# Kernel optimization log

Hardware: AMD Instinct MI355X
Metric: run time of the kernel (lower is better)

The kernel has to match this reference:

```python
import jax, jax.numpy as jnp
import numpy as np
from jax import lax

NUM_HEADS = 6
LN_EPS = 1e-5


def _ln(x, g, b):
    mu = jnp.mean(x, axis=-1, keepdims=True)
    var = jnp.mean(jnp.square(x - mu), axis=-1, keepdims=True)
    return (x - mu) * jax.lax.rsqrt(var + LN_EPS) * g + b


def _gelu(x):
    return jax.nn.gelu(x, approximate=False)


def setup_inputs() -> dict:
    key = jax.random.key(0)
    ks = jax.random.split(key, 16)
    B, N, C = 16, 1025, 384
    hid = 4 * C  # 1536
    k3 = 3  # depthwise kernel size
    s = 0.02
    rn = lambda k, shape: (jax.random.normal(k, shape, jnp.float32) * s)
    return {
        "x": jax.random.normal(ks[0], (B, N, C), jnp.float32),
        "ln1_g": jnp.ones((C,), jnp.float32),
        "ln1_b": jnp.zeros((C,), jnp.float32),
        "qkv_w": rn(ks[1], (3 * C, C)),
        "proj_w": rn(ks[2], (C, C)),
        "proj_b": jnp.zeros((C,), jnp.float32),
        "ln2_g": jnp.ones((C,), jnp.float32),
        "ln2_b": jnp.zeros((C,), jnp.float32),
        "conv1_w": rn(ks[3], (hid, C)),          # 1x1 conv as matrix
        "conv1_b": jnp.zeros((hid,), jnp.float32),
        "conv2_w": rn(ks[4], (hid, 1, k3, k3)),   # depthwise OIHW
        "conv2_b": jnp.zeros((hid,), jnp.float32),
        "conv3_w": rn(ks[5], (C, hid)),           # 1x1 conv as matrix
        "conv3_b": jnp.zeros((C,), jnp.float32),
        "bn1_s": jnp.ones((hid,), jnp.float32), "bn1_b": jnp.zeros((hid,), jnp.float32),
        "bn2_s": jnp.ones((hid,), jnp.float32), "bn2_b": jnp.zeros((hid,), jnp.float32),
        "bn3_s": jnp.ones((C,), jnp.float32), "bn3_b": jnp.zeros((C,), jnp.float32),
        "comp_w": rn(ks[6], (C // 4, C)), "comp_b": jnp.zeros((C // 4,), jnp.float32),
        "exc_w": rn(ks[7], (C, C // 4)), "exc_b": jnp.zeros((C,), jnp.float32),
    }


def _block(x, ln1_g, ln1_b, qkv_w, proj_w, proj_b, ln2_g, ln2_b,
           conv1_w, conv1_b, conv2_w, conv2_b, conv3_w, conv3_b,
           bn1_s, bn1_b, bn2_s, bn2_b, bn3_s, bn3_b,
           comp_w, comp_b, exc_w, exc_b):
    B, N, C = x.shape
    Hh = NUM_HEADS
    hd = C // Hh
    S = int(np.sqrt(N - 1))

    # ---- Attention (manual softmax(QK^T)V) ----
    h = _ln(x, ln1_g, ln1_b)
    qkv = jnp.einsum('bnc,dc->bnd', h, qkv_w).reshape(B, N, 3, Hh, hd)
    qkv = qkv.transpose(2, 0, 3, 1, 4)  # [3,B,H,N,hd]
    q, k, v = qkv[0], qkv[1], qkv[2]
    attn = jax.nn.softmax(jnp.einsum('bhqd,bhkd->bhqk', q, k) * (hd ** -0.5), axis=-1)
    o = jnp.einsum('bhqk,bhkd->bhqd', attn, v).transpose(0, 2, 1, 3).reshape(B, N, C)
    o = o @ proj_w.T + proj_b
    x = x + o

    # ---- DAFF FFN (conv + BN(eval affine) + GELU + SE gating on cls) ----
    h2 = _ln(x, ln2_g, ln2_b)
    cls_tok, tok = h2[:, :1], h2[:, 1:]
    t = tok.reshape(B, S, S, C).transpose(0, 3, 1, 2)  # NCHW
    hid = conv1_w.shape[0]
    y = jnp.einsum('bchw,oc->bohw', t, conv1_w) + conv1_b[None, :, None, None]
    y = y * bn1_s[None, :, None, None] + bn1_b[None, :, None, None]
    y = _gelu(y)
    shortcut = y
    y = lax.conv_general_dilated(y, conv2_w, (1, 1), 'SAME',
                                 feature_group_count=hid,
                                 dimension_numbers=('NCHW', 'OIHW', 'NCHW'))
    y = y + conv2_b[None, :, None, None]
    y = y * bn2_s[None, :, None, None] + bn2_b[None, :, None, None]
    y = shortcut + _gelu(y)
    y = jnp.einsum('bchw,oc->bohw', y, conv3_w) + conv3_b[None, :, None, None]
    y = y * bn3_s[None, :, None, None] + bn3_b[None, :, None, None]
    # SE gate on cls token
    w = jnp.mean(y, axis=(2, 3)).reshape(B, 1, C)
    w = _gelu(w @ comp_w.T + comp_b) @ exc_w.T + exc_b
    cls_out = cls_tok * w
    tok_out = y.reshape(B, C, S * S).transpose(0, 2, 1)
    out = jnp.concatenate([cls_out, tok_out], axis=1)
    return x + out


def reference(x, ln1_g, ln1_b, qkv_w, proj_w, proj_b, ln2_g, ln2_b,
              conv1_w, conv1_b, conv2_w, conv2_b, conv3_w, conv3_b,
              bn1_s, bn1_b, bn2_s, bn2_b, bn3_s, bn3_b,
              comp_w, comp_b, exc_w, exc_b):
    return _block(x, ln1_g, ln1_b, qkv_w, proj_w, proj_b, ln2_g, ln2_b,
                  conv1_w, conv1_b, conv2_w, conv2_b, conv3_w, conv3_b,
                  bn1_s, bn1_b, bn2_s, bn2_b, bn3_s, bn3_b,
                  comp_w, comp_b, exc_w, exc_b)
```

## Files before the change

kernel.cpp:

```cpp
#include <hip/hip_runtime.h>
#include <math.h>

#define DI __device__ __forceinline__

namespace {

constexpr int B_ = 16;
constexpr int N_ = 1025;
constexpr int C_ = 384;
constexpr int H_ = 6;
constexpr int HD_ = 64;
constexpr int HID_ = 1536;
constexpr int P_ = 1024;
constexpr int MTOK = B_ * P_;
constexpr int MALL = B_ * N_;
constexpr int NPAD = 1088;
constexpr long long AF = (long long)MALL * C_;

constexpr int NQKV = 3 * C_ * C_;
constexpr int NPROJ = C_ * C_;
constexpr int NC1 = HID_ * C_;
constexpr int NC3 = C_ * HID_;
constexpr int NW2 = HID_ * 9;
constexpr int T1 = NQKV, T2 = T1 + NPROJ, T3 = T2 + NC1, T4 = T3 + NC3;
constexpr int T5 = T4 + NW2, T6 = T5 + HID_;

typedef __attribute__((ext_vector_type(4))) float f32x4;
typedef __attribute__((ext_vector_type(8))) short bf16x8;

DI float gelu_f(float x) { return 0.5f * x * (1.0f + erff(x * 0.7071067811865475f)); }

DI float us2f(unsigned short u) {
  union { unsigned int i; float f; } c; c.i = ((unsigned)u) << 16; return c.f;
}
DI unsigned short f2us(float f) {
  union { float f; unsigned int i; } c; c.f = f;
  unsigned int r = c.i + 0x7FFF + ((c.i >> 16) & 1);
  return (unsigned short)(r >> 16);
}
DI unsigned short f2us_trunc(float f) {
  union { float f; unsigned int i; } c; c.f = f;
  return (unsigned short)(c.i >> 16);
}
DI void bf8_to_f(const uint4 v, float* f) {
  const unsigned int u[4] = {v.x, v.y, v.z, v.w};
#pragma unroll
  for (int t = 0; t < 4; t++) {
    union { unsigned int i; float fl; } lo, hi;
    lo.i = (u[t] & 0xffffu) << 16;
    hi.i = u[t] & 0xffff0000u;
    f[2 * t] = lo.fl; f[2 * t + 1] = hi.fl;
  }
}
DI uint4 f_to_bf8(const float* f) {
  unsigned int w[4];
#pragma unroll
  for (int t = 0; t < 4; t++)
    w[t] = (unsigned)f2us(f[2 * t]) | ((unsigned)f2us(f[2 * t + 1]) << 16);
  return make_uint4(w[0], w[1], w[2], w[3]);
}

DI void gl2lds16(const unsigned short* g, unsigned short* l) {
  __builtin_amdgcn_global_load_lds(
      (const __attribute__((address_space(1))) void*)g,
      (__attribute__((address_space(3))) void*)l, 16, 0, 0);
}

__global__ __launch_bounds__(256) void cvtall_kernel(
    const float* __restrict__ qkv_w, const float* __restrict__ proj_w,
    const float* __restrict__ conv1_w, const float* __restrict__ conv3_w,
    const float* __restrict__ conv2_w, const float* __restrict__ c2b,
    const float* __restrict__ s2, const float* __restrict__ b2,
    unsigned short* __restrict__ dst16, float* __restrict__ Bc)
{
  const int idx = blockIdx.x * 256 + threadIdx.x;
  if (idx < T1)      dst16[idx] = f2us(qkv_w[idx]);
  else if (idx < T2) dst16[idx] = f2us(proj_w[idx - T1]);
  else if (idx < T3) dst16[idx] = f2us(conv1_w[idx - T2]);
  else if (idx < T4) dst16[idx] = f2us(conv3_w[idx - T3]);
  else if (idx < T5) {
    const int r = idx - T4, tap = r / HID_, c = r % HID_;
    dst16[idx] = f2us(conv2_w[c * 9 + tap] * s2[c]);
  } else if (idx < T6) {
    const int c = idx - T5;
    Bc[c] = c2b[c] * s2[c] + b2[c];
  }
}

__global__ __launch_bounds__(256) void lnw_kernel(
    const float* __restrict__ x, const float* __restrict__ g,
    const float* __restrict__ b, unsigned short* __restrict__ out,
    float* __restrict__ cls_out, int nrows)
{
  const int row = blockIdx.x * 4 + (threadIdx.x >> 6);
  if (row >= nrows) return;
  const int lane = threadIdx.x & 63;
  const float* xr = x + (long long)row * C_;
  float v[6];
#pragma unroll
  for (int i = 0; i < 6; i++) v[i] = xr[lane + 64 * i];
  float s = 0.f, q = 0.f;
#pragma unroll
  for (int i = 0; i < 6; i++) { s += v[i]; q += v[i] * v[i]; }
#pragma unroll
  for (int m = 1; m < 64; m <<= 1) {
    s += __shfl_xor(s, m, 64);
    q += __shfl_xor(q, m, 64);
  }
  const float mean = s * (1.0f / C_);
  const float var  = q * (1.0f / C_) - mean * mean;
  const float rstd = rsqrtf(var + 1e-5f);
  unsigned short* orow = out + (long long)row * C_;
  const bool iscls = (cls_out != nullptr) && (row % N_) == 0;
  float* cr = iscls ? cls_out + (long long)(row / N_) * C_ : nullptr;
#pragma unroll
  for (int i = 0; i < 6; i++) {
    const int c = lane + 64 * i;
    const float r = (v[i] - mean) * rstd * g[c] + b[c];
    orow[c] = f2us(r);
    if (iscls) cr[c] = r;
  }
}

__global__ __launch_bounds__(256) void vtrans_kernel(
    const unsigned short* __restrict__ v, unsigned short* __restrict__ vt)
{
  __shared__ unsigned short t[64][72];
  const int bh = blockIdx.x, nt = blockIdx.y;
  const int n0 = nt * 64;
  const int tid = threadIdx.x;
  {
    const int nl = tid >> 2;
    const int dc = (tid & 3) * 16;
    const int gn = n0 + nl;
    uint4 a = make_uint4(0u,0u,0u,0u), b = make_uint4(0u,0u,0u,0u);
    if (gn < N_) {
      const unsigned short* p = v + ((long long)bh * N_ + gn) * HD_ + dc;
      a = *(const uint4*)p; b = *(const uint4*)(p + 8);
    }
    *(uint4*)&t[nl][dc] = a;
    *(uint4*)&t[nl][dc + 8] = b;
  }
  __syncthreads();
  {
    const int dl = tid >> 2;
    const int nc = (tid & 3) * 16;
    unsigned short tmp[16];
#pragma unroll
    for (int i = 0; i < 16; i++) tmp[i] = t[nc + i][dl];
    unsigned short* p = vt + ((long long)bh * HD_ + dl) * NPAD + n0 + nc;
    *(uint4*)p = *(uint4*)&tmp[0];
    *(uint4*)(p + 8) = *(uint4*)&tmp[8];
  }
}

enum { GM_QKV = 0, GM_PROJ = 1, GM_CONV1 = 2, GM_CONV3 = 3 };

template <int MODE, int K>
__global__ __launch_bounds__(256) void mgemm_kernel(
    const unsigned short* __restrict__ A, const unsigned short* __restrict__ W,
    void* __restrict__ o0, void* __restrict__ o1, void* __restrict__ o2,
    const float* __restrict__ e0, const float* __restrict__ e1,
    const float* __restrict__ e2, int M)
{
  __shared__ unsigned short As[128][64];
  __shared__ unsigned short Bs[128][64];
  const int m0 = blockIdx.x * 128, n0 = blockIdx.y * 128;
  if (m0 >= M) return;
  const int tid = threadIdx.x;
  const int lane = tid & 63, wv = tid >> 6;
  const int lane15 = lane & 15, quad = lane >> 4;
  const int wm = (wv >> 1) * 64, wn = (wv & 1) * 64;

  const unsigned short* agp[4];
  const unsigned short* bgp[4];
#pragma unroll
  for (int t = 0; t < 4; t++) {
    const int lr = wv * 32 + t * 8 + (lane >> 3);
    const int chunk = (lane & 7) ^ (lr & 7);
    int gm = m0 + lr;
    if (gm > M - 1) gm = M - 1;
    long long arow = gm;
    if constexpr (MODE == GM_CONV1) arow = (long long)(gm >> 10) * N_ + 1 + (gm & 1023);
    agp[t] = A + arow * K + chunk * 8;
    bgp[t] = W + (long long)(n0 + lr) * K + chunk * 8;
  }

  f32x4 acc[4][4];
#pragma unroll
  for (int i = 0; i < 4; i++)
#pragma unroll
    for (int j = 0; j < 4; j++) acc[i][j] = (f32x4)0.f;

  const int xsel = lane15 & 7;
  for (int k0 = 0; k0 < K; k0 += 64) {
    __syncthreads();
#pragma unroll
    for (int t = 0; t < 4; t++) {
      gl2lds16(agp[t] + k0, &As[wv * 32 + t * 8][0]);
      gl2lds16(bgp[t] + k0, &Bs[wv * 32 + t * 8][0]);
    }
    __syncthreads();
#pragma unroll
    for (int kh = 0; kh < 2; kh++) {
      bf16x8 af[4], bfr[4];
#pragma unroll
      for (int i = 0; i < 4; i++)
        af[i] = *(const bf16x8*)&As[wm + i * 16 + lane15][((kh * 4 + quad) ^ xsel) * 8];
#pragma unroll
      for (int j = 0; j < 4; j++)
        bfr[j] = *(const bf16x8*)&Bs[wn + j * 16 + lane15][((kh * 4 + quad) ^ xsel) * 8];
#pragma unroll
      for (int i = 0; i < 4; i++)
#pragma unroll
        for (int j = 0; j < 4; j++)
          acc[i][j] = __builtin_amdgcn_mfma_f32_16x16x32_bf16(af[i], bfr[j], acc[i][j], 0, 0, 0);
    }
  }
#pragma unroll
  for (int i = 0; i < 4; i++) {
#pragma unroll
    for (int r = 0; r < 4; r++) {
      const int m = m0 + wm + i * 16 + quad * 4 + r;
      if (m >= M) continue;
#pragma unroll
      for (int j = 0; j < 4; j++) {
        const int n = n0 + wn + j * 16 + lane15;
        const float val = acc[i][j][r];
        if constexpr (MODE == GM_QKV) {
          const int which = n / C_, rr = n % C_, hh = rr >> 6, e = rr & 63;
          const int b = m / N_, nn = m % N_;
          unsigned short* dst = (unsigned short*)((which == 0) ? o0 : ((which == 1) ? o1 : o2));
          const float sval = (which == 0) ? val * 0.18033688f : val;
          dst[(((long long)b * H_ + hh) * N_ + nn) * HD_ + e] = f2us(sval);
        } else if constexpr (MODE == GM_PROJ) {
          ((float*)o0)[(long long)m * C_ + n] = val + e0[(long long)m * C_ + n] + e1[n];
        } else if constexpr (MODE == GM_CONV1) {
          ((unsigned short*)o0)[(long long)m * HID_ + n] =
              f2us(gelu_f((val + e0[n]) * e1[n] + e2[n]));
        } else {
          const float val2 = (val + e0[n]) * e1[n] + e2[n];
          ((float*)o0)[(long long)m * C_ + n] = val2;
          const int bb = m >> 10, pp = m & 1023;
          const long long orow = ((long long)bb * N_ + 1 + pp) * C_ + n;
          ((float*)o1)[orow] = ((const float*)o2)[orow] + val2;
        }
      }
    }
  }
}

__global__ __launch_bounds__(256) void fattn_kernel(
    const unsigned short* __restrict__ q, const unsigned short* __restrict__ k,
    const unsigned short* __restrict__ vt, unsigned short* __restrict__ o)
{
  __shared__ unsigned short Ks[64][64];
  __shared__ unsigned short Vt[64][64];
  __shared__ unsigned short Ps[4][16][72];
  const int tid = threadIdx.x;
  const int lane = tid & 63, wv = tid >> 6;
  const int lane15 = lane & 15, quad = lane >> 4;
  const int bh = blockIdx.x, qt = blockIdx.y;
  const long long headoff = (long long)bh * N_;
  const int q0 = qt * 64 + wv * 16;

  const long long qrow = headoff + q0 + lane15;
  const bf16x8 aq0 = *(const bf16x8*)(q + qrow * HD_ + quad * 8);
  const bf16x8 aq1 = *(const bf16x8*)(q + qrow * HD_ + 32 + quad * 8);

  const unsigned short* kgp[2];
  const unsigned short* vgp[2];
#pragma unroll
  for (int t = 0; t < 2; t++) {
    const int row = wv * 16 + t * 8 + (lane >> 3);
    const int ch = (lane & 7) ^ (row & 7);
    kgp[t] = k + (headoff + row) * HD_ + ch * 8;
    vgp[t] = vt + ((long long)bh * HD_ + row) * NPAD + ch * 8;
  }

  f32x4 O[4];
  float l_r[4] = {0.f, 0.f, 0.f, 0.f};
#pragma unroll
  for (int n = 0; n < 4; n++) O[n] = (f32x4)0.f;

  const int xsel = lane15 & 7;
  for (int kt = 0; kt < 17; kt++) {
    const int kt0 = kt * 64;
    __syncthreads();
#pragma unroll
    for (int t = 0; t < 2; t++) {
      gl2lds16(kgp[t] + (long long)kt0 * HD_, &Ks[wv * 16 + t * 8][0]);
      gl2lds16(vgp[t] + kt0, &Vt[wv * 16 + t * 8][0]);
    }
    __syncthreads();

    f32x4 S[4];
#pragma unroll
    for (int n = 0; n < 4; n++) {
      S[n] = (f32x4)0.f;
      const bf16x8 b0 = *(const bf16x8*)&Ks[n * 16 + lane15][(quad ^ xsel) * 8];
      S[n] = __builtin_amdgcn_mfma_f32_16x16x32_bf16(aq0, b0, S[n], 0, 0, 0);
      const bf16x8 b1 = *(const bf16x8*)&Ks[n * 16 + lane15][((4 + quad) ^ xsel) * 8];
      S[n] = __builtin_amdgcn_mfma_f32_16x16x32_bf16(aq1, b1, S[n], 0, 0, 0);
    }
    if (kt == 16) {
#pragma unroll
      for (int n = 0; n < 4; n++) {
        if ((kt0 + n * 16 + lane15) >= N_)
#pragma unroll
          for (int r = 0; r < 4; r++) S[n][r] = -1e30f;
      }
    }
#pragma unroll
    for (int n = 0; n < 4; n++)
#pragma unroll
      for (int r = 0; r < 4; r++) {
        const float p = exp2f(S[n][r]);
        l_r[r] += p;
        Ps[wv][quad * 4 + r][n * 16 + lane15] = f2us_trunc(p);
      }
#pragma unroll
    for (int half = 0; half < 2; half++) {
      const bf16x8 ap = *(const bf16x8*)&Ps[wv][lane15][half * 32 + quad * 8];
#pragma unroll
      for (int n = 0; n < 4; n++) {
        const bf16x8 bv =
            *(const bf16x8*)&Vt[n * 16 + lane15][(((half * 4 + quad)) ^ xsel) * 8];
        O[n] = __builtin_amdgcn_mfma_f32_16x16x32_bf16(ap, bv, O[n], 0, 0, 0);
      }
    }
  }
#pragma unroll
  for (int msk = 1; msk < 16; msk <<= 1)
#pragma unroll
    for (int r = 0; r < 4; r++) l_r[r] += __shfl_xor(l_r[r], msk, 64);

  const int b = bh / H_, hh = bh % H_;
#pragma unroll
  for (int r = 0; r < 4; r++) {
    const int gq = q0 + quad * 4 + r;
    if (gq < N_) {
      const float inv = 1.0f / l_r[r];
#pragma unroll
      for (int n = 0; n < 4; n++)
        o[((long long)b * N_ + gq) * C_ + hh * HD_ + n * 16 + lane15] = f2us(O[n][r] * inv);
    }
  }
}

__global__ __launch_bounds__(192) void dwconv_kernel(
    const unsigned short* __restrict__ y1, const unsigned short* __restrict__ w2s,
    const float* __restrict__ Bc, unsigned short* __restrict__ y2)
{
  const int jp = blockIdx.x & 15;
  const int i  = (blockIdx.x >> 4) & 31;
  const int b  = blockIdx.x >> 9;
  const int j0 = jp * 2;
  const int cb = threadIdx.x << 3;

  float wf[9][8];
#pragma unroll
  for (int tap = 0; tap < 9; tap++) {
    const uint4 wv = *(const uint4*)(w2s + tap * HID_ + cb);
    bf8_to_f(wv, wf[tap]);
  }
  float acc0[8] = {}, acc1[8] = {};
  float sh0[8], sh1[8];
#pragma unroll
  for (int di = -1; di <= 1; di++) {
    const int ii = i + di;
    if (ii < 0 || ii > 31) continue;
    const long long rowbase = ((long long)b * P_ + ii * 32) * HID_ + cb;
#pragma unroll
    for (int dj = -1; dj <= 2; dj++) {
      const int jj = j0 + dj;
      if (jj < 0 || jj > 31) continue;
      const uint4 dv = *(const uint4*)(y1 + rowbase + (long long)jj * HID_);
      float df[8]; bf8_to_f(dv, df);
      if (dj <= 1) {
        const int tap = (di + 1) * 3 + (dj + 1);
#pragma unroll
        for (int t = 0; t < 8; t++) acc0[t] += df[t] * wf[tap][t];
      }
      if (dj >= 0) {
        const int tap = (di + 1) * 3 + dj;
#pragma unroll
        for (int t = 0; t < 8; t++) acc1[t] += df[t] * wf[tap][t];
      }
      if (di == 0 && dj == 0) {
#pragma unroll
        for (int t = 0; t < 8; t++) sh0[t] = df[t];
      }
      if (di == 0 && dj == 1) {
#pragma unroll
        for (int t = 0; t < 8; t++) sh1[t] = df[t];
      }
    }
  }
  const float4 bc0 = *(const float4*)(Bc + cb);
  const float4 bc1 = *(const float4*)(Bc + cb + 4);
  const float bcv[8] = {bc0.x, bc0.y, bc0.z, bc0.w, bc1.x, bc1.y, bc1.z, bc1.w};
  float of0[8], of1[8];
#pragma unroll
  for (int t = 0; t < 8; t++) {
    of0[t] = sh0[t] + gelu_f(acc0[t] + bcv[t]);
    of1[t] = sh1[t] + gelu_f(acc1[t] + bcv[t]);
  }
  const long long tok0 = ((long long)b * P_ + i * 32 + j0) * HID_ + cb;
  *(uint4*)(y2 + tok0) = f_to_bf8(of0);
  *(uint4*)(y2 + tok0 + HID_) = f_to_bf8(of1);
}

__global__ __launch_bounds__(384) void pool_kernel(const float* __restrict__ y3,
                                                   float* __restrict__ w0p)
{
  const int b = blockIdx.x, chunk = blockIdx.y;
  const int c = threadIdx.x;
  float s = 0.f;
  for (int p = chunk * 64; p < chunk * 64 + 64; p++)
    s += y3[((long long)b * P_ + p) * C_ + c];
  w0p[((long long)b * 16 + chunk) * C_ + c] = s;
}

__global__ __launch_bounds__(128) void se_kernel(
    const float* __restrict__ w0p, const float* __restrict__ cw,
    const float* __restrict__ cb, const float* __restrict__ ew,
    const float* __restrict__ eb, float* __restrict__ wfin)
{
  __shared__ float wm[384];
  __shared__ float t1[96];
  const int b = blockIdx.x, t = threadIdx.x;
  for (int c = t; c < 384; c += 128) {
    float s = 0.f;
    for (int ch = 0; ch < 16; ch++) s += w0p[((long long)b * 16 + ch) * C_ + c];
    wm[c] = s * (1.0f / 1024.0f);
  }
  __syncthreads();
  if (t < 96) {
    float s = cb[t];
    for (int c = 0; c < 384; c++) s += wm[c] * cw[t * 384 + c];
    t1[t] = gelu_f(s);
  }
  __syncthreads();
  for (int c = t; c < 384; c += 128) {
    float s = eb[c];
    for (int j = 0; j < 96; j++) s += t1[j] * ew[c * 96 + j];
    wfin[(long long)b * C_ + c] = s;
  }
}

__global__ __launch_bounds__(256) void clsfix_kernel(
    const float* __restrict__ x2, const float* __restrict__ cls,
    const float* __restrict__ wfin, float* __restrict__ out)
{
  const int idx = blockIdx.x * 256 + threadIdx.x;
  if (idx >= B_ * C_) return;
  const int b = idx / C_, c = idx % C_;
  const long long row = (long long)b * N_ * C_ + c;
  out[row] = x2[row] + cls[idx] * wfin[idx];
}

}

extern "C" void kernel_launch(void* const* d_in, const int* in_sizes, int n_in,
                              void* d_out, int out_size, void* d_ws, size_t ws_size,
                              hipStream_t stream)
{
  const float* x       = (const float*)d_in[0];
  const float* ln1_g   = (const float*)d_in[1];
  const float* ln1_b   = (const float*)d_in[2];
  const float* qkv_w   = (const float*)d_in[3];
  const float* proj_w  = (const float*)d_in[4];
  const float* proj_b  = (const float*)d_in[5];
  const float* ln2_g   = (const float*)d_in[6];
  const float* ln2_b   = (const float*)d_in[7];
  const float* conv1_w = (const float*)d_in[8];
  const float* conv1_b = (const float*)d_in[9];
  const float* conv2_w = (const float*)d_in[10];
  const float* conv2_b = (const float*)d_in[11];
  const float* conv3_w = (const float*)d_in[12];
  const float* conv3_b = (const float*)d_in[13];
  const float* bn1_s   = (const float*)d_in[14];
  const float* bn1_b   = (const float*)d_in[15];
  const float* bn2_s   = (const float*)d_in[16];
  const float* bn2_b   = (const float*)d_in[17];
  const float* bn3_s   = (const float*)d_in[18];
  const float* bn3_b   = (const float*)d_in[19];
  const float* comp_w  = (const float*)d_in[20];
  const float* comp_b  = (const float*)d_in[21];
  const float* exc_w   = (const float*)d_in[22];
  const float* exc_b   = (const float*)d_in[23];

  char* wsb = (char*)d_ws;
  const size_t RA = 50331648, RB = 50331648, RC = 25190400;
  const size_t tailbytes = (size_t)T5 * 2 +
                           (size_t)(HID_ + B_ * C_ + B_ * 16 * C_ + B_ * C_) * 4;
  const size_t needed = RA + RB + RC + tailbytes;
  if (ws_size < needed) return;

  unsigned short* qb  = (unsigned short*)wsb;
  unsigned short* kb  = qb + AF;
  unsigned short* vb  = kb + AF;
  unsigned short* h2b = (unsigned short*)wsb;
  unsigned short* y2  = (unsigned short*)wsb;
  char* rb = wsb + RA;
  unsigned short* hb  = (unsigned short*)rb;
  unsigned short* o16 = (unsigned short*)rb;
  unsigned short* y1  = (unsigned short*)rb;
  float* y3           = (float*)rb;
  unsigned short* vtb = (unsigned short*)(wsb + RA + RB);
  float* x2 = (float*)(wsb + RA + RB);
  unsigned short* w16 = (unsigned short*)(wsb + RA + RB + RC);
  unsigned short* wqkv16  = w16;
  unsigned short* wproj16 = w16 + T1;
  unsigned short* wc116   = w16 + T2;
  unsigned short* wc316   = w16 + T3;
  unsigned short* w2s     = w16 + T4;
  float* Bc   = (float*)(w16 + T5);
  float* cls  = Bc + HID_;
  float* w0p  = cls + B_ * C_;
  float* wfin = w0p + B_ * 16 * C_;

  cvtall_kernel<<<(T6 + 255) / 256, 256, 0, stream>>>(
      qkv_w, proj_w, conv1_w, conv3_w, conv2_w, conv2_b, bn2_s, bn2_b, w16, Bc);
  lnw_kernel<<<(MALL + 3) / 4, 256, 0, stream>>>(x, ln1_g, ln1_b, hb, nullptr, MALL);
  mgemm_kernel<GM_QKV, 384><<<dim3(136, 9), 256, 0, stream>>>(
      hb, wqkv16, qb, kb, vb, nullptr, nullptr, nullptr, MALL);
  vtrans_kernel<<<dim3(B_ * H_, 17), 256, 0, stream>>>(vb, vtb);
  fattn_kernel<<<dim3(B_ * H_, 17), 256, 0, stream>>>(qb, kb, vtb, o16);
  mgemm_kernel<GM_PROJ, 384><<<dim3(136, 3), 256, 0, stream>>>(
      o16, wproj16, x2, nullptr, nullptr, x, proj_b, nullptr, MALL);
  lnw_kernel<<<(MALL + 3) / 4, 256, 0, stream>>>(x2, ln2_g, ln2_b, h2b, cls, MALL);
  mgemm_kernel<GM_CONV1, 384><<<dim3(128, 12), 256, 0, stream>>>(
      h2b, wc116, y1, nullptr, nullptr, conv1_b, bn1_s, bn1_b, MTOK);
  dwconv_kernel<<<B_ * 32 * 16, 192, 0, stream>>>(y1, w2s, Bc, y2);
  mgemm_kernel<GM_CONV3, 1536><<<dim3(128, 3), 256, 0, stream>>>(
      y2, wc316, y3, (float*)d_out, x2, conv3_b, bn3_s, bn3_b, MTOK);
  pool_kernel<<<dim3(B_, 16), 384, 0, stream>>>(y3, w0p);
  se_kernel<<<B_, 128, 0, stream>>>(w0p, comp_w, comp_b, exc_w, exc_b, wfin);
  clsfix_kernel<<<(B_ * C_ + 255) / 256, 256, 0, stream>>>(x2, cls, wfin, (float*)d_out);
}
```

Before: 423.8 us.

## Double-buffer K/V tiles in flash attention with 8-wave 128-query blocks

The attention kernel now uses 512 threads per block covering 128 query rows. K and V tiles are double-buffered in LDS: the next tile is prefetched before computing on the current one, so there is one barrier per iteration instead of two. Wave priority is raised around the MFMA sections. Query rows past the end are clamped for loading. The larger block shares each K/V tile across twice as many queries, but the grid shrinks to 9 query tiles with some wasted rows in the last tile, and LDS use per block grows.

```diff
diff --git a/kernel.cpp b/kernel.cpp
--- a/kernel.cpp
+++ b/kernel.cpp
@@ -250,33 +250,30 @@
   }
 }
 
-__global__ __launch_bounds__(256) void fattn_kernel(
+__global__ __launch_bounds__(512) void fattn_kernel(
     const unsigned short* __restrict__ q, const unsigned short* __restrict__ k,
     const unsigned short* __restrict__ vt, unsigned short* __restrict__ o)
 {
-  __shared__ unsigned short Ks[64][64];
-  __shared__ unsigned short Vt[64][64];
-  __shared__ unsigned short Ps[4][16][72];
+  __shared__ unsigned short Ks[2][64][64];
+  __shared__ unsigned short Vt[2][64][64];
+  __shared__ unsigned short Ps[8][16][72];
   const int tid = threadIdx.x;
   const int lane = tid & 63, wv = tid >> 6;
   const int lane15 = lane & 15, quad = lane >> 4;
   const int bh = blockIdx.x, qt = blockIdx.y;
   const long long headoff = (long long)bh * N_;
-  const int q0 = qt * 64 + wv * 16;
-
-  const long long qrow = headoff + q0 + lane15;
+  const int q0 = qt * 128 + wv * 16;
+
+  int gq0 = q0 + lane15;
+  if (gq0 > N_ - 1) gq0 = N_ - 1;
+  const long long qrow = headoff + gq0;
   const bf16x8 aq0 = *(const bf16x8*)(q + qrow * HD_ + quad * 8);
   const bf16x8 aq1 = *(const bf16x8*)(q + qrow * HD_ + 32 + quad * 8);
 
-  const unsigned short* kgp[2];
-  const unsigned short* vgp[2];
-#pragma unroll
-  for (int t = 0; t < 2; t++) {
-    const int row = wv * 16 + t * 8 + (lane >> 3);
-    const int ch = (lane & 7) ^ (row & 7);
-    kgp[t] = k + (headoff + row) * HD_ + ch * 8;
-    vgp[t] = vt + ((long long)bh * HD_ + row) * NPAD + ch * 8;
-  }
+  const int srow = wv * 8 + (lane >> 3);
+  const int ch = (lane & 7) ^ (srow & 7);
+  const unsigned short* kgp = k + (headoff + srow) * HD_ + ch * 8;
+  const unsigned short* vgp = vt + ((long long)bh * HD_ + srow) * NPAD + ch * 8;
 
   f32x4 O[4];
   float l_r[4] = {0.f, 0.f, 0.f, 0.f};
@@ -284,29 +281,34 @@
   for (int n = 0; n < 4; n++) O[n] = (f32x4)0.f;
 
   const int xsel = lane15 & 7;
+
+  gl2lds16(kgp, &Ks[0][wv * 8][0]);
+  gl2lds16(vgp, &Vt[0][wv * 8][0]);
+  __syncthreads();
+
   for (int kt = 0; kt < 17; kt++) {
-    const int kt0 = kt * 64;
-    __syncthreads();
-#pragma unroll
-    for (int t = 0; t < 2; t++) {
-      gl2lds16(kgp[t] + (long long)kt0 * HD_, &Ks[wv * 16 + t * 8][0]);
-      gl2lds16(vgp[t] + kt0, &Vt[wv * 16 + t * 8][0]);
-    }
-    __syncthreads();
+    const int cur = kt & 1;
+    if (kt < 16) {
+      const long long koff = (long long)(kt + 1) * 64;
+      gl2lds16(kgp + koff * HD_, &Ks[cur ^ 1][wv * 8][0]);
+      gl2lds16(vgp + koff, &Vt[cur ^ 1][wv * 8][0]);
+    }
 
     f32x4 S[4];
+    __builtin_amdgcn_s_setprio(1);
 #pragma unroll
     for (int n = 0; n < 4; n++) {
       S[n] = (f32x4)0.f;
-      const bf16x8 b0 = *(const bf16x8*)&Ks[n * 16 + lane15][(quad ^ xsel) * 8];
+      const bf16x8 b0 = *(const bf16x8*)&Ks[cur][n * 16 + lane15][(quad ^ xsel) * 8];
       S[n] = __builtin_amdgcn_mfma_f32_16x16x32_bf16(aq0, b0, S[n], 0, 0, 0);
-      const bf16x8 b1 = *(const bf16x8*)&Ks[n * 16 + lane15][((4 + quad) ^ xsel) * 8];
+      const bf16x8 b1 = *(const bf16x8*)&Ks[cur][n * 16 + lane15][((4 + quad) ^ xsel) * 8];
       S[n] = __builtin_amdgcn_mfma_f32_16x16x32_bf16(aq1, b1, S[n], 0, 0, 0);
     }
+    __builtin_amdgcn_s_setprio(0);
     if (kt == 16) {
 #pragma unroll
       for (int n = 0; n < 4; n++) {
-        if ((kt0 + n * 16 + lane15) >= N_)
+        if ((kt * 64 + n * 16 + lane15) >= N_)
 #pragma unroll
           for (int r = 0; r < 4; r++) S[n][r] = -1e30f;
       }
@@ -319,16 +321,19 @@
         l_r[r] += p;
         Ps[wv][quad * 4 + r][n * 16 + lane15] = f2us_trunc(p);
       }
+    __builtin_amdgcn_s_setprio(1);
 #pragma unroll
     for (int half = 0; half < 2; half++) {
       const bf16x8 ap = *(const bf16x8*)&Ps[wv][lane15][half * 32 + quad * 8];
 #pragma unroll
       for (int n = 0; n < 4; n++) {
         const bf16x8 bv =
-            *(const bf16x8*)&Vt[n * 16 + lane15][(((half * 4 + quad)) ^ xsel) * 8];
+            *(const bf16x8*)&Vt[cur][n * 16 + lane15][(((half * 4 + quad)) ^ xsel) * 8];
         O[n] = __builtin_amdgcn_mfma_f32_16x16x32_bf16(ap, bv, O[n], 0, 0, 0);
       }
     }
+    __builtin_amdgcn_s_setprio(0);
+    __syncthreads();
   }
 #pragma unroll
   for (int msk = 1; msk < 16; msk <<= 1)
@@ -527,7 +532,7 @@
   mgemm_kernel<GM_QKV, 384><<<dim3(136, 9), 256, 0, stream>>>(
       hb, wqkv16, qb, kb, vb, nullptr, nullptr, nullptr, MALL);
   vtrans_kernel<<<dim3(B_ * H_, 17), 256, 0, stream>>>(vb, vtb);
-  fattn_kernel<<<dim3(B_ * H_, 17), 256, 0, stream>>>(qb, kb, vtb, o16);
+  fattn_kernel<<<dim3(B_ * H_, 9), 512, 0, stream>>>(qb, kb, vtb, o16);
   mgemm_kernel<GM_PROJ, 384><<<dim3(136, 3), 256, 0, stream>>>(
       o16, wproj16, x2, nullptr, nullptr, x, proj_b, nullptr, MALL);
   lnw_kernel<<<(MALL + 3) / 4, 256, 0, stream>>>(x2, ln2_g, ln2_b, h2b, cls, MALL);
```

Result: faster. 414.9 us (-2.1%).
